# Kernel tuning notes

Measured on AMD Instinct MI355X. Metric: run time of the kernel, lower is better.

The kernel has to match this reference:

```python
import jax, jax.numpy as jnp
import numpy as np

N = 100000
E = 1600000
NFEAT = 128
NHID = 128
NCLASS = 10


def setup_inputs() -> dict:
    key = jax.random.key(0)
    ks = jax.random.split(key, 12)
    x = jax.random.normal(ks[0], (N, NFEAT), dtype=jnp.float32)
    edge_index = jax.random.randint(ks[1], (2, E), 0, N, dtype=jnp.int64)
    s = 0.05
    W1 = jax.random.normal(ks[2], (NFEAT, NHID), dtype=jnp.float32) * s
    b1 = jnp.zeros((NHID,), dtype=jnp.float32)
    W2 = jax.random.normal(ks[3], (NHID, NHID), dtype=jnp.float32) * s
    b2 = jnp.zeros((NHID,), dtype=jnp.float32)
    W3 = jax.random.normal(ks[4], (NHID, NHID), dtype=jnp.float32) * s
    b3 = jnp.zeros((NHID,), dtype=jnp.float32)
    Wl = jax.random.normal(ks[5], (NHID, NCLASS), dtype=jnp.float32) * s
    bl = jnp.zeros((NCLASS,), dtype=jnp.float32)
    return {"x": x, "edge_index": edge_index, "W1": W1, "b1": b1,
            "W2": W2, "b2": b2, "W3": W3, "b3": b3, "Wl": Wl, "bl": bl}


def _gcn_norm(edge_index, num_nodes):
    # PyG gcn_norm with add_self_loops=True and unit edge weights.
    loops = jnp.arange(num_nodes, dtype=edge_index.dtype)
    src = jnp.concatenate([edge_index[0], loops])  # [E+N]
    dst = jnp.concatenate([edge_index[1], loops])
    ones = jnp.ones(src.shape[0], dtype=jnp.float32)
    deg = jax.ops.segment_sum(ones, dst, num_segments=num_nodes)
    dis = jax.lax.rsqrt(deg)  # deg >= 1 due to self-loops
    norm = dis[src] * dis[dst]  # [E+N]
    return src, dst, norm


def _gcn_conv(h, src, dst, norm, W, b, num_nodes):
    h = h @ W                                   # [N, out]
    msg = h[src] * norm[:, None]                # gather + edge scaling
    out = jax.ops.segment_sum(msg, dst, num_segments=num_nodes)
    return out + b


def reference(x, edge_index, W1, b1, W2, b2, W3, b3, Wl, bl):
    src, dst, norm = _gcn_norm(edge_index, N)
    h = jax.nn.relu(_gcn_conv(x, src, dst, norm, W1, b1, N))
    h = jax.nn.relu(_gcn_conv(h, src, dst, norm, W2, b2, N))
    h = _gcn_conv(h, src, dst, norm, W3, b3, N)
    logits = h @ Wl + bl                        # dropout is identity (eval / p=0)
    return jax.nn.log_softmax(logits, axis=1)
```

## Files before the change

### kernel.cpp

```cpp
#include <hip/hip_runtime.h>

#define NFEAT 128
#define NCLS  10
#define NCP   16
#define BROW  512
#define BINC  4096

static inline size_t alignup(size_t x) { return (x + 255) & ~size_t(255); }

__device__ __forceinline__ ushort f2bf(float f) {
  uint x = __float_as_uint(f);
  return (ushort)((x + 0x7fffu + ((x >> 16) & 1u)) >> 16);
}
__device__ __forceinline__ float bf2f(ushort u) {
  return __uint_as_float(((uint)u) << 16);
}

typedef short bf16x8 __attribute__((ext_vector_type(8)));
typedef float f32x4 __attribute__((ext_vector_type(4)));


__global__ __launch_bounds__(256) void bucket_hist(const int* __restrict__ dst,
                                                   int* __restrict__ bkt_cnt,
                                                   int e, int nbkt) {
  __shared__ int hist[256];
  for (int t = threadIdx.x; t < nbkt; t += 256) hist[t] = 0;
  __syncthreads();
  int i = blockIdx.x * 256 + threadIdx.x;
  int stride = gridDim.x * 256;
  for (; i < e; i += stride) atomicAdd(&hist[dst[i] >> 9], 1);
  __syncthreads();
  for (int t = threadIdx.x; t < nbkt; t += 256)
    if (hist[t]) atomicAdd(&bkt_cnt[t], hist[t]);
}

__global__ __launch_bounds__(256) void bkt_scan(const int* __restrict__ bkt_cnt,
                                                int* __restrict__ bkt_off,
                                                int* __restrict__ gfrontier,
                                                int n, int nbkt) {
  __shared__ int sbuf[256];
  const int t = threadIdx.x;
  int x = 0;
  if (t < nbkt) {
    int lo = t << 9;
    int nodes = n - lo; if (nodes > BROW) nodes = BROW;
    x = bkt_cnt[t] + nodes;
  }
  sbuf[t] = x;
  __syncthreads();
  for (int off = 1; off < 256; off <<= 1) {
    int v = (t >= off) ? sbuf[t - off] : 0;
    __syncthreads();
    sbuf[t] += v;
    __syncthreads();
  }
  if (t < nbkt) { bkt_off[t] = sbuf[t] - x; gfrontier[t] = sbuf[t] - x; }
  if (t == nbkt - 1) bkt_off[nbkt] = sbuf[t];
}

__global__ __launch_bounds__(256) void bin_items(const int* __restrict__ ei,
                                                 int nE, int total, int nbkt,
                                                 int* __restrict__ gfrontier,
                                                 uint* __restrict__ binned) {
  __shared__ int hist[256];
  __shared__ int loff[256];
  __shared__ int gbase[256];
  __shared__ int sbuf[256];
  __shared__ int2 st[BINC];
  const int t = threadIdx.x;
  const int chunk0 = blockIdx.x * BINC;
  for (int q = t; q < nbkt; q += 256) hist[q] = 0;
  __syncthreads();
  for (int j = t; j < BINC; j += 256) {
    int i = chunk0 + j;
    if (i < total) {
      int d = (i < nE) ? ei[nE + i] : (i - nE);
      atomicAdd(&hist[d >> 9], 1);
    }
  }
  __syncthreads();
  int x = (t < nbkt) ? hist[t] : 0;
  sbuf[t] = x;
  __syncthreads();
  for (int off = 1; off < 256; off <<= 1) {
    int v = (t >= off) ? sbuf[t - off] : 0;
    __syncthreads();
    sbuf[t] += v;
    __syncthreads();
  }
  loff[t] = sbuf[t] - x;
  gbase[t] = (t < nbkt && x > 0) ? atomicAdd(&gfrontier[t], x) : 0;
  __syncthreads();
  hist[t] = loff[t];
  __syncthreads();
  for (int j = t; j < BINC; j += 256) {
    int i = chunk0 + j;
    if (i < total) {
      int s, d;
      if (i < nE) { s = ei[i]; d = ei[nE + i]; }
      else        { s = i - nE; d = s; }
      int p = atomicAdd(&hist[d >> 9], 1);
      st[p] = make_int2(s, d);
    }
  }
  __syncthreads();
  int M = total - chunk0; if (M > BINC) M = BINC;
  for (int j = t; j < M; j += 256) {
    int2 it = st[j];
    int b = it.y >> 9;
    uint pk = (uint)it.x | ((uint)(it.y & 511) << 17);
    binned[gbase[b] + (j - loff[b])] = pk;
  }
}

__global__ __launch_bounds__(512) void bucket_finalize(const uint* __restrict__ binned,
                                                       const int* __restrict__ bkt_off,
                                                       int* __restrict__ row_ptr,
                                                       float* __restrict__ dis,
                                                       int* __restrict__ ev,
                                                       int n, int nbkt) {
  __shared__ int hist[BROW];
  __shared__ int sbuf[BROW];
  __shared__ int pre[BROW];
  __shared__ int front[BROW];
  const int b = blockIdx.x;
  const int t = threadIdx.x;
  const int row0 = b << 9;
  const int beg = bkt_off[b], end = bkt_off[b + 1];
  hist[t] = 0; front[t] = 0;
  __syncthreads();
  for (int j = beg + t; j < end; j += BROW)
    atomicAdd(&hist[binned[j] >> 17], 1);
  __syncthreads();
  const int x = hist[t];
  const int v = row0 + t;
  if (v < n) dis[v] = rsqrtf((float)x);
  sbuf[t] = x;
  __syncthreads();
  for (int off = 1; off < BROW; off <<= 1) {
    int val = (t >= off) ? sbuf[t - off] : 0;
    __syncthreads();
    sbuf[t] += val;
    __syncthreads();
  }
  pre[t] = sbuf[t] - x;
  if (v < n) row_ptr[v] = beg + pre[t];
  if (b == nbkt - 1 && t == 0) row_ptr[n] = end;
  __syncthreads();
  for (int j = beg + t; j < end; j += BROW) {
    uint pk = binned[j];
    int dl = pk >> 17;
    int slot = atomicAdd(&front[dl], 1);
    ev[beg + pre[dl] + slot] = (int)(pk & 0x1FFFFu);
  }
}


__global__ __launch_bounds__(256) void prep_all(const float* __restrict__ W1,
                                                const float* __restrict__ W2,
                                                const float* __restrict__ W3,
                                                const float* __restrict__ Wl,
                                                const float* __restrict__ b3,
                                                const float* __restrict__ bl,
                                                ushort* __restrict__ Wt1,
                                                ushort* __restrict__ Wt2,
                                                float* __restrict__ Wf,
                                                float* __restrict__ bf) {
  const int bid = blockIdx.x;
  if (bid < 8) {
    int t = bid * 256 + threadIdx.x;
    int r = t >> 4, c = t & 15;
    float s = 0.f;
    if (c < NCLS) {
      for (int k = 0; k < NFEAT; ++k) s += W3[r * NFEAT + k] * Wl[k * NCLS + c];
    }
    Wf[t] = s;
    if (t < NCP) {
      float sb = 0.f;
      if (t < NCLS) {
        sb = bl[t];
        for (int k = 0; k < NFEAT; ++k) sb += b3[k] * Wl[k * NCLS + t];
      }
      bf[t] = sb;
    }
  } else {
    int t = (bid - 8) * 256 + threadIdx.x;
    int u = t & 16383;
    int n = u >> 7, k = u & 127;
    if (t < 16384) Wt1[n * NFEAT + k] = f2bf(W1[k * NFEAT + n]);
    else           Wt2[n * NFEAT + k] = f2bf(W2[k * NFEAT + n]);
  }
}


template<bool BF16IN>
__global__ __launch_bounds__(256) void gemm_mfma(const float* __restrict__ A,
                                                 const ushort* __restrict__ Ab,
                                                 const ushort* __restrict__ Wt,
                                                 const float* __restrict__ dis,
                                                 ushort* __restrict__ Cb, int nrows) {
  __shared__ __align__(16) ushort Asm[64 * NFEAT];
  const int tid = threadIdx.x;
  const int row0 = blockIdx.x * 64;
  {
    const int m = tid >> 2;
    const int kc = (tid & 3) * 32;
    const int gr = row0 + m;
    int4 u[4];
    if (BF16IN) {
      if (gr < nrows) {
        const ushort* p = Ab + (size_t)gr * NFEAT + kc;
        u[0] = *(const int4*)(p + 0);
        u[1] = *(const int4*)(p + 8);
        u[2] = *(const int4*)(p + 16);
        u[3] = *(const int4*)(p + 24);
      } else {
        u[0] = u[1] = u[2] = u[3] = make_int4(0, 0, 0, 0);
      }
    } else {
      float4 f[8];
      if (gr < nrows) {
        #pragma unroll
        for (int q = 0; q < 8; ++q)
          f[q] = *(const float4*)&A[(size_t)gr * NFEAT + kc + q * 4];
      } else {
        #pragma unroll
        for (int q = 0; q < 8; ++q) f[q] = make_float4(0.f, 0.f, 0.f, 0.f);
      }
      #pragma unroll
      for (int q = 0; q < 4; ++q) {
        union { ushort us[8]; int4 v; } pk;
        const float* fp = (const float*)&f[q * 2];
        #pragma unroll
        for (int j = 0; j < 8; ++j) pk.us[j] = f2bf(fp[j]);
        u[q] = pk.v;
      }
    }
    #pragma unroll
    for (int q = 0; q < 4; ++q) {
      int byte = (m * 256 + (kc + q * 8) * 2) ^ ((m & 7) << 4);
      *(int4*)((char*)Asm + byte) = u[q];
    }
  }
  __syncthreads();
  const int wave = tid >> 6;
  const int lane = tid & 63;
  const int m0 = wave * 16;
  bf16x8 afr[4];
  #pragma unroll
  for (int ks = 0; ks < 4; ++ks) {
    int m = m0 + (lane & 15);
    int kk = ks * 32 + (lane >> 4) * 8;
    int byte = (m * 256 + kk * 2) ^ ((m & 7) << 4);
    afr[ks] = *(const bf16x8*)((const char*)Asm + byte);
  }
  f32x4 acc[8];
  #pragma unroll
  for (int c = 0; c < 8; ++c) acc[c] = (f32x4){0.f, 0.f, 0.f, 0.f};
  #pragma unroll
  for (int c = 0; c < 8; ++c) {
    #pragma unroll
    for (int ks = 0; ks < 4; ++ks) {
      int n = c * 16 + (lane & 15);
      int kk = ks * 32 + (lane >> 4) * 8;
      bf16x8 bfr = *(const bf16x8*)&Wt[n * NFEAT + kk];
      acc[c] = __builtin_amdgcn_mfma_f32_16x16x32_bf16(afr[ks], bfr, acc[c], 0, 0, 0);
    }
  }
  const int gr_base = row0 + m0 + (lane >> 4) * 4;
  float dr[4];
  #pragma unroll
  for (int r = 0; r < 4; ++r)
    dr[r] = (gr_base + r < nrows) ? dis[gr_base + r] : 0.f;
  #pragma unroll
  for (int c = 0; c < 8; ++c) {
    #pragma unroll
    for (int r = 0; r < 4; ++r) {
      int gr = gr_base + r;
      if (gr < nrows)
        Cb[(size_t)gr * NFEAT + c * 16 + (lane & 15)] = f2bf(acc[c][r] * dr[r]);
    }
  }
}


__global__ __launch_bounds__(256) void aggregate(const ushort* __restrict__ hw,
                                                 const int* __restrict__ row_ptr,
                                                 const int* __restrict__ ev,
                                                 const float* __restrict__ dis,
                                                 const float* __restrict__ bias,
                                                 ushort* __restrict__ outb,
                                                 int relu, int n) {
  const int wave = threadIdx.x >> 6;
  const int lane = threadIdx.x & 63;
  const int v = blockIdx.x * 4 + wave;
  if (v >= n) return;
  const int beg = row_ptr[v], end = row_ptr[v + 1];
  const int half = lane >> 5;
  const int hl = lane & 31;
  float4 acc = make_float4(0.f, 0.f, 0.f, 0.f);
  int e = beg + half;
  for (; e + 6 < end; e += 8) {
    int s0 = ev[e];
    int s1 = ev[e + 2];
    int s2 = ev[e + 4];
    int s3 = ev[e + 6];
    ushort4 q0 = *(const ushort4*)&hw[(size_t)s0 * NFEAT + hl * 4];
    ushort4 q1 = *(const ushort4*)&hw[(size_t)s1 * NFEAT + hl * 4];
    ushort4 q2 = *(const ushort4*)&hw[(size_t)s2 * NFEAT + hl * 4];
    ushort4 q3 = *(const ushort4*)&hw[(size_t)s3 * NFEAT + hl * 4];
    acc.x += bf2f(q0.x) + bf2f(q1.x) + bf2f(q2.x) + bf2f(q3.x);
    acc.y += bf2f(q0.y) + bf2f(q1.y) + bf2f(q2.y) + bf2f(q3.y);
    acc.z += bf2f(q0.z) + bf2f(q1.z) + bf2f(q2.z) + bf2f(q3.z);
    acc.w += bf2f(q0.w) + bf2f(q1.w) + bf2f(q2.w) + bf2f(q3.w);
  }
  for (; e < end; e += 2) {
    int s = ev[e];
    ushort4 q = *(const ushort4*)&hw[(size_t)s * NFEAT + hl * 4];
    acc.x += bf2f(q.x); acc.y += bf2f(q.y);
    acc.z += bf2f(q.z); acc.w += bf2f(q.w);
  }
  acc.x += __shfl_xor(acc.x, 32);
  acc.y += __shfl_xor(acc.y, 32);
  acc.z += __shfl_xor(acc.z, 32);
  acc.w += __shfl_xor(acc.w, 32);
  if (half == 0) {
    float dv = dis[v];
    float4 b = *(const float4*)&bias[hl * 4];
    acc.x = fmaf(acc.x, dv, b.x); acc.y = fmaf(acc.y, dv, b.y);
    acc.z = fmaf(acc.z, dv, b.z); acc.w = fmaf(acc.w, dv, b.w);
    if (relu) {
      acc.x = fmaxf(acc.x, 0.f); acc.y = fmaxf(acc.y, 0.f);
      acc.z = fmaxf(acc.z, 0.f); acc.w = fmaxf(acc.w, 0.f);
    }
    union { ushort us[4]; uint2 q2; } pk;
    pk.us[0] = f2bf(acc.x); pk.us[1] = f2bf(acc.y);
    pk.us[2] = f2bf(acc.z); pk.us[3] = f2bf(acc.w);
    *(uint2*)&outb[(size_t)v * NFEAT + hl * 4] = pk.q2;
  }
}


__global__ __launch_bounds__(256) void gemm_small(const ushort* __restrict__ Ab,
                                                  const float* __restrict__ Wf,
                                                  const float* __restrict__ dis,
                                                  ushort* __restrict__ Gb, int n) {
  __shared__ float Ws[NFEAT * NCP];
  for (int i = threadIdx.x; i < NFEAT * NCP; i += 256) Ws[i] = Wf[i];
  __syncthreads();
  const int v = blockIdx.x * 256 + threadIdx.x;
  if (v >= n) return;
  float acc[NCP];
  #pragma unroll
  for (int c = 0; c < NCP; ++c) acc[c] = 0.f;
  #pragma unroll
  for (int p = 0; p < 8; ++p) {
    union { ushort us[16]; int4 q[2]; } a;
    const ushort* pl = Ab + (size_t)v * NFEAT + p * 16;
    a.q[0] = *(const int4*)pl;
    a.q[1] = *(const int4*)(pl + 8);
    #pragma unroll
    for (int j = 0; j < 16; ++j) {
      float av = bf2f(a.us[j]);
      int k = p * 16 + j;
      #pragma unroll
      for (int cq = 0; cq < NCP; cq += 4) {
        float4 w = *(const float4*)&Ws[k * NCP + cq];
        acc[cq + 0] += av * w.x;
        acc[cq + 1] += av * w.y;
        acc[cq + 2] += av * w.z;
        acc[cq + 3] += av * w.w;
      }
    }
  }
  const float dv = dis[v];
  union { ushort us[16]; int4 q[2]; } pk;
  #pragma unroll
  for (int c = 0; c < NCP; ++c) pk.us[c] = f2bf(acc[c] * dv);
  *(int4*)&Gb[(size_t)v * NCP + 0] = pk.q[0];
  *(int4*)&Gb[(size_t)v * NCP + 8] = pk.q[1];
}


__global__ __launch_bounds__(256) void agg_logits(const ushort* __restrict__ Gb,
                                                  const int* __restrict__ row_ptr,
                                                  const int* __restrict__ ev,
                                                  const float* __restrict__ dis,
                                                  const float* __restrict__ bf,
                                                  float* __restrict__ out, int n) {
  const int wave = threadIdx.x >> 6;
  const int lane = threadIdx.x & 63;
  const int v = blockIdx.x * 4 + wave;
  if (v >= n) return;
  const int beg = row_ptr[v], end = row_ptr[v + 1];
  const int g = lane >> 4;
  const int f = lane & 15;
  float acc = 0.f;
  int e = beg + g;
  for (; e + 4 < end; e += 8) {
    int s0 = ev[e];
    int s1 = ev[e + 4];
    acc += bf2f(Gb[(size_t)s0 * NCP + f]) + bf2f(Gb[(size_t)s1 * NCP + f]);
  }
  for (; e < end; e += 4) {
    acc += bf2f(Gb[(size_t)ev[e] * NCP + f]);
  }
  acc += __shfl_xor(acc, 16);
  acc += __shfl_xor(acc, 32);
  float logit = dis[v] * acc + bf[f];
  float pv = (f < NCLS) ? logit : -INFINITY;
  float m = pv;
  #pragma unroll
  for (int s = 8; s >= 1; s >>= 1) m = fmaxf(m, __shfl_xor(m, s));
  float ex = (f < NCLS) ? expf(logit - m) : 0.f;
  float ssum = ex;
  #pragma unroll
  for (int s = 8; s >= 1; s >>= 1) ssum += __shfl_xor(ssum, s);
  float lse = m + logf(ssum);
  if (g == 0 && f < NCLS) out[(size_t)v * NCLS + f] = logit - lse;
}


extern "C" void kernel_launch(void* const* d_in, const int* in_sizes, int n_in,
                              void* d_out, int out_size, void* d_ws, size_t ws_size,
                              hipStream_t stream) {
  const float* x  = (const float*)d_in[0];
  const int*   ei = (const int*)d_in[1];
  const float* W1 = (const float*)d_in[2];
  const float* b1 = (const float*)d_in[3];
  const float* W2 = (const float*)d_in[4];
  const float* b2 = (const float*)d_in[5];
  const float* W3 = (const float*)d_in[6];
  const float* b3 = (const float*)d_in[7];
  const float* Wl = (const float*)d_in[8];
  const float* bl = (const float*)d_in[9];
  float* out = (float*)d_out;

  const int nN = in_sizes[0] / NFEAT;
  const int nE = in_sizes[1] / 2;
  const int total = nN + nE;
  const int nbkt = (nN + BROW - 1) >> 9;
  const int nbBin = (total + BINC - 1) / BINC;

  char* ws = (char*)d_ws;
  int*    bkt_cnt = (int*)ws;     ws += alignup(256 * 4);
  int*    bkt_off = (int*)ws;     ws += alignup(257 * 4);
  int*    gfront  = (int*)ws;     ws += alignup(256 * 4);
  int*    row_ptr = (int*)ws;     ws += alignup((size_t)(nN + 1) * 4);
  float*  dis     = (float*)ws;   ws += alignup((size_t)nN * 4);
  float*  Wf      = (float*)ws;   ws += alignup((size_t)NFEAT * NCP * 4);
  float*  bfv     = (float*)ws;   ws += alignup((size_t)NCP * 4);
  ushort* Wt1     = (ushort*)ws;  ws += alignup((size_t)NFEAT * NFEAT * 2);
  ushort* Wt2     = (ushort*)ws;  ws += alignup((size_t)NFEAT * NFEAT * 2);
  uint*   binned  = (uint*)ws;    ws += alignup((size_t)total * 4);
  int*    ev      = (int*)ws;     ws += alignup((size_t)total * 4);
  ushort* hb      = (ushort*)ws;  ws += alignup((size_t)nN * NFEAT * 2);
  ushort* hbA     = (ushort*)ws;  ws += alignup((size_t)nN * NFEAT * 2);
  ushort* Gb      = (ushort*)ws;  ws += alignup((size_t)nN * NCP * 2);

  hipMemsetAsync(bkt_cnt, 0, 256 * sizeof(int), stream);
  bucket_hist<<<512, 256, 0, stream>>>(ei + nE, bkt_cnt, nE, nbkt);
  bkt_scan<<<1, 256, 0, stream>>>(bkt_cnt, bkt_off, gfront, nN, nbkt);
  bin_items<<<nbBin, 256, 0, stream>>>(ei, nE, total, nbkt, gfront, binned);
  bucket_finalize<<<nbkt, BROW, 0, stream>>>(binned, bkt_off, row_ptr, dis, ev, nN, nbkt);

  prep_all<<<136, 256, 0, stream>>>(W1, W2, W3, Wl, b3, bl, Wt1, Wt2, Wf, bfv);

  const int gemm_grid = (nN + 63) / 64;
  const int node_grid = (nN + 3) / 4;

  gemm_mfma<false><<<gemm_grid, 256, 0, stream>>>(x, nullptr, Wt1, dis, hb, nN);
  aggregate<<<node_grid, 256, 0, stream>>>(hb, row_ptr, ev, dis, b1, hbA, 1, nN);
  gemm_mfma<true><<<gemm_grid, 256, 0, stream>>>(nullptr, hbA, Wt2, dis, hb, nN);
  aggregate<<<node_grid, 256, 0, stream>>>(hb, row_ptr, ev, dis, b2, hbA, 1, nN);
  gemm_small<<<(nN + 255) / 256, 256, 0, stream>>>(hbA, Wf, dis, Gb, nN);
  agg_logits<<<node_grid, 256, 0, stream>>>(Gb, row_ptr, ev, dis, bfv, out, nN);
}
```

Measured before the change: 353.2 us.

## Fuse weight prep into histogram, use wave-shuffle scans, unroll aggregation by eight

Merges the weight-prep kernel into the edge histogram kernel as extra blocks, which removes one launch. The shared-memory Hillis-Steele scans in bkt_scan, bin_items and bucket_finalize become wavefront shuffle scans plus a small cross-wave fix-up, cutting the number of barriers. The aggregate kernel gains a 16-edge-per-iteration main loop so each lane keeps eight gathers in flight. The extra unrolling raises register pressure, and the gain depends on how much time launches and scans take compared with the gathers.

Measured after the change: 341.2 us. 1.04x faster.

```diff
diff --git a/kernel.cpp b/kernel.cpp
--- a/kernel.cpp
+++ b/kernel.cpp
@@ -20,14 +20,52 @@
 typedef float f32x4 __attribute__((ext_vector_type(4)));
 
 
-__global__ __launch_bounds__(256) void bucket_hist(const int* __restrict__ dst,
-                                                   int* __restrict__ bkt_cnt,
-                                                   int e, int nbkt) {
+__global__ __launch_bounds__(256) void hist_prep(const int* __restrict__ dst,
+                                                 int* __restrict__ bkt_cnt,
+                                                 int e, int nbkt,
+                                                 const float* __restrict__ W1,
+                                                 const float* __restrict__ W2,
+                                                 const float* __restrict__ W3,
+                                                 const float* __restrict__ Wl,
+                                                 const float* __restrict__ b3,
+                                                 const float* __restrict__ bl,
+                                                 ushort* __restrict__ Wt1,
+                                                 ushort* __restrict__ Wt2,
+                                                 float* __restrict__ Wf,
+                                                 float* __restrict__ bf) {
+  const int bid = blockIdx.x;
+  if (bid >= 512) {
+    const int pb = bid - 512;
+    if (pb < 8) {
+      int t = pb * 256 + threadIdx.x;
+      int r = t >> 4, c = t & 15;
+      float s = 0.f;
+      if (c < NCLS) {
+        for (int k = 0; k < NFEAT; ++k) s += W3[r * NFEAT + k] * Wl[k * NCLS + c];
+      }
+      Wf[t] = s;
+      if (t < NCP) {
+        float sb = 0.f;
+        if (t < NCLS) {
+          sb = bl[t];
+          for (int k = 0; k < NFEAT; ++k) sb += b3[k] * Wl[k * NCLS + t];
+        }
+        bf[t] = sb;
+      }
+    } else {
+      int t = (pb - 8) * 256 + threadIdx.x;
+      int u = t & 16383;
+      int n = u >> 7, k = u & 127;
+      if (t < 16384) Wt1[n * NFEAT + k] = f2bf(W1[k * NFEAT + n]);
+      else           Wt2[n * NFEAT + k] = f2bf(W2[k * NFEAT + n]);
+    }
+    return;
+  }
   __shared__ int hist[256];
   for (int t = threadIdx.x; t < nbkt; t += 256) hist[t] = 0;
   __syncthreads();
-  int i = blockIdx.x * 256 + threadIdx.x;
-  int stride = gridDim.x * 256;
+  int i = bid * 256 + threadIdx.x;
+  const int stride = 512 * 256;
   for (; i < e; i += stride) atomicAdd(&hist[dst[i] >> 9], 1);
   __syncthreads();
   for (int t = threadIdx.x; t < nbkt; t += 256)
@@ -38,24 +76,30 @@
                                                 int* __restrict__ bkt_off,
                                                 int* __restrict__ gfrontier,
                                                 int n, int nbkt) {
-  __shared__ int sbuf[256];
+  __shared__ int wsum[4];
   const int t = threadIdx.x;
+  const int lane = t & 63, wv = t >> 6;
   int x = 0;
   if (t < nbkt) {
     int lo = t << 9;
     int nodes = n - lo; if (nodes > BROW) nodes = BROW;
     x = bkt_cnt[t] + nodes;
   }
-  sbuf[t] = x;
-  __syncthreads();
-  for (int off = 1; off < 256; off <<= 1) {
-    int v = (t >= off) ? sbuf[t - off] : 0;
-    __syncthreads();
-    sbuf[t] += v;
-    __syncthreads();
-  }
-  if (t < nbkt) { bkt_off[t] = sbuf[t] - x; gfrontier[t] = sbuf[t] - x; }
-  if (t == nbkt - 1) bkt_off[nbkt] = sbuf[t];
+  int xs = x;
+  #pragma unroll
+  for (int off = 1; off < 64; off <<= 1) {
+    int y = __shfl_up(xs, off);
+    if (lane >= off) xs += y;
+  }
+  if (lane == 63) wsum[wv] = xs;
+  __syncthreads();
+  int add = 0;
+  if (wv > 0) add += wsum[0];
+  if (wv > 1) add += wsum[1];
+  if (wv > 2) add += wsum[2];
+  int incl = xs + add;
+  if (t < nbkt) { bkt_off[t] = incl - x; gfrontier[t] = incl - x; }
+  if (t == nbkt - 1) bkt_off[nbkt] = incl;
 }
 
 __global__ __launch_bounds__(256) void bin_items(const int* __restrict__ ei,
@@ -65,9 +109,10 @@
   __shared__ int hist[256];
   __shared__ int loff[256];
   __shared__ int gbase[256];
-  __shared__ int sbuf[256];
+  __shared__ int wsum[4];
   __shared__ int2 st[BINC];
   const int t = threadIdx.x;
+  const int lane = t & 63, wv = t >> 6;
   const int chunk0 = blockIdx.x * BINC;
   for (int q = t; q < nbkt; q += 256) hist[q] = 0;
   __syncthreads();
@@ -80,17 +125,20 @@
   }
   __syncthreads();
   int x = (t < nbkt) ? hist[t] : 0;
-  sbuf[t] = x;
-  __syncthreads();
-  for (int off = 1; off < 256; off <<= 1) {
-    int v = (t >= off) ? sbuf[t - off] : 0;
-    __syncthreads();
-    sbuf[t] += v;
-    __syncthreads();
-  }
-  loff[t] = sbuf[t] - x;
+  int xs = x;
+  #pragma unroll
+  for (int off = 1; off < 64; off <<= 1) {
+    int y = __shfl_up(xs, off);
+    if (lane >= off) xs += y;
+  }
+  if (lane == 63) wsum[wv] = xs;
+  __syncthreads();
+  int add = 0;
+  if (wv > 0) add += wsum[0];
+  if (wv > 1) add += wsum[1];
+  if (wv > 2) add += wsum[2];
+  loff[t] = xs + add - x;
   gbase[t] = (t < nbkt && x > 0) ? atomicAdd(&gfrontier[t], x) : 0;
-  __syncthreads();
   hist[t] = loff[t];
   __syncthreads();
   for (int j = t; j < BINC; j += 256) {
@@ -120,11 +168,12 @@
                                                        int* __restrict__ ev,
                                                        int n, int nbkt) {
   __shared__ int hist[BROW];
-  __shared__ int sbuf[BROW];
   __shared__ int pre[BROW];
   __shared__ int front[BROW];
+  __shared__ int wsum[8];
   const int b = blockIdx.x;
   const int t = threadIdx.x;
+  const int lane = t & 63, wv = t >> 6;
   const int row0 = b << 9;
   const int beg = bkt_off[b], end = bkt_off[b + 1];
   hist[t] = 0; front[t] = 0;
@@ -135,15 +184,19 @@
   const int x = hist[t];
   const int v = row0 + t;
   if (v < n) dis[v] = rsqrtf((float)x);
-  sbuf[t] = x;
-  __syncthreads();
-  for (int off = 1; off < BROW; off <<= 1) {
-    int val = (t >= off) ? sbuf[t - off] : 0;
-    __syncthreads();
-    sbuf[t] += val;
-    __syncthreads();
-  }
-  pre[t] = sbuf[t] - x;
+  int xs = x;
+  #pragma unroll
+  for (int off = 1; off < 64; off <<= 1) {
+    int y = __shfl_up(xs, off);
+    if (lane >= off) xs += y;
+  }
+  if (lane == 63) wsum[wv] = xs;
+  __syncthreads();
+  int add = 0;
+  #pragma unroll
+  for (int w = 0; w < 7; ++w)
+    if (w < wv) add += wsum[w];
+  pre[t] = xs + add - x;
   if (v < n) row_ptr[v] = beg + pre[t];
   if (b == nbkt - 1 && t == 0) row_ptr[n] = end;
   __syncthreads();
@@ -152,43 +205,6 @@
     int dl = pk >> 17;
     int slot = atomicAdd(&front[dl], 1);
     ev[beg + pre[dl] + slot] = (int)(pk & 0x1FFFFu);
-  }
-}
-
-
-__global__ __launch_bounds__(256) void prep_all(const float* __restrict__ W1,
-                                                const float* __restrict__ W2,
-                                                const float* __restrict__ W3,
-                                                const float* __restrict__ Wl,
-                                                const float* __restrict__ b3,
-                                                const float* __restrict__ bl,
-                                                ushort* __restrict__ Wt1,
-                                                ushort* __restrict__ Wt2,
-                                                float* __restrict__ Wf,
-                                                float* __restrict__ bf) {
-  const int bid = blockIdx.x;
-  if (bid < 8) {
-    int t = bid * 256 + threadIdx.x;
-    int r = t >> 4, c = t & 15;
-    float s = 0.f;
-    if (c < NCLS) {
-      for (int k = 0; k < NFEAT; ++k) s += W3[r * NFEAT + k] * Wl[k * NCLS + c];
-    }
-    Wf[t] = s;
-    if (t < NCP) {
-      float sb = 0.f;
-      if (t < NCLS) {
-        sb = bl[t];
-        for (int k = 0; k < NFEAT; ++k) sb += b3[k] * Wl[k * NCLS + t];
-      }
-      bf[t] = sb;
-    }
-  } else {
-    int t = (bid - 8) * 256 + threadIdx.x;
-    int u = t & 16383;
-    int n = u >> 7, k = u & 127;
-    if (t < 16384) Wt1[n * NFEAT + k] = f2bf(W1[k * NFEAT + n]);
-    else           Wt2[n * NFEAT + k] = f2bf(W2[k * NFEAT + n]);
   }
 }
 
@@ -300,6 +316,32 @@
   const int hl = lane & 31;
   float4 acc = make_float4(0.f, 0.f, 0.f, 0.f);
   int e = beg + half;
+  for (; e + 14 < end; e += 16) {
+    int s0 = ev[e];
+    int s1 = ev[e + 2];
+    int s2 = ev[e + 4];
+    int s3 = ev[e + 6];
+    int s4 = ev[e + 8];
+    int s5 = ev[e + 10];
+    int s6 = ev[e + 12];
+    int s7 = ev[e + 14];
+    ushort4 q0 = *(const ushort4*)&hw[(size_t)s0 * NFEAT + hl * 4];
+    ushort4 q1 = *(const ushort4*)&hw[(size_t)s1 * NFEAT + hl * 4];
+    ushort4 q2 = *(const ushort4*)&hw[(size_t)s2 * NFEAT + hl * 4];
+    ushort4 q3 = *(const ushort4*)&hw[(size_t)s3 * NFEAT + hl * 4];
+    ushort4 q4 = *(const ushort4*)&hw[(size_t)s4 * NFEAT + hl * 4];
+    ushort4 q5 = *(const ushort4*)&hw[(size_t)s5 * NFEAT + hl * 4];
+    ushort4 q6 = *(const ushort4*)&hw[(size_t)s6 * NFEAT + hl * 4];
+    ushort4 q7 = *(const ushort4*)&hw[(size_t)s7 * NFEAT + hl * 4];
+    acc.x += (bf2f(q0.x) + bf2f(q1.x) + bf2f(q2.x) + bf2f(q3.x))
+           + (bf2f(q4.x) + bf2f(q5.x) + bf2f(q6.x) + bf2f(q7.x));
+    acc.y += (bf2f(q0.y) + bf2f(q1.y) + bf2f(q2.y) + bf2f(q3.y))
+           + (bf2f(q4.y) + bf2f(q5.y) + bf2f(q6.y) + bf2f(q7.y));
+    acc.z += (bf2f(q0.z) + bf2f(q1.z) + bf2f(q2.z) + bf2f(q3.z))
+           + (bf2f(q4.z) + bf2f(q5.z) + bf2f(q6.z) + bf2f(q7.z));
+    acc.w += (bf2f(q0.w) + bf2f(q1.w) + bf2f(q2.w) + bf2f(q3.w))
+           + (bf2f(q4.w) + bf2f(q5.w) + bf2f(q6.w) + bf2f(q7.w));
+  }
   for (; e + 6 < end; e += 8) {
     int s0 = ev[e];
     int s1 = ev[e + 2];
@@ -459,12 +501,11 @@
   ushort* Gb      = (ushort*)ws;  ws += alignup((size_t)nN * NCP * 2);
 
   hipMemsetAsync(bkt_cnt, 0, 256 * sizeof(int), stream);
-  bucket_hist<<<512, 256, 0, stream>>>(ei + nE, bkt_cnt, nE, nbkt);
+  hist_prep<<<648, 256, 0, stream>>>(ei + nE, bkt_cnt, nE, nbkt,
+                                     W1, W2, W3, Wl, b3, bl, Wt1, Wt2, Wf, bfv);
   bkt_scan<<<1, 256, 0, stream>>>(bkt_cnt, bkt_off, gfront, nN, nbkt);
   bin_items<<<nbBin, 256, 0, stream>>>(ei, nE, total, nbkt, gfront, binned);
   bucket_finalize<<<nbkt, BROW, 0, stream>>>(binned, bkt_off, row_ptr, dis, ev, nN, nbkt);
-
-  prep_all<<<136, 256, 0, stream>>>(W1, W2, W3, Wl, b3, bl, Wt1, Wt2, Wf, bfv);
 
   const int gemm_grid = (nN + 63) / 64;
   const int node_grid = (nN + 3) / 4;
```
